# Kernel tuning notes

Hardware: AMD Instinct MI355X
Metric: run time of the kernel (lower is better)

The kernel has to match this reference:

```python
import jax, jax.numpy as jnp
import numpy as np

N = 50000      # nodes
E = 800000     # edges
NIN = 512      # input features
NHID = 128     # hidden
NCLS = 64      # classes


def setup_inputs() -> dict:
    key = jax.random.key(0)
    k0, k1, k2, k3 = jax.random.split(key, 4)
    x = jax.random.normal(k0, (N, NIN), dtype=jnp.float32)
    edge_index = jax.random.randint(k1, (2, E), 0, N, dtype=jnp.int64)
    # Glorot-style init for GCNConv linear weights (bias starts at zero in PyG)
    W1 = jax.random.normal(k2, (NIN, NHID), dtype=jnp.float32) * (1.0 / np.sqrt(NIN))
    W2 = jax.random.normal(k3, (NHID, NCLS), dtype=jnp.float32) * (1.0 / np.sqrt(NHID))
    b1 = jnp.zeros((NHID,), dtype=jnp.float32)
    b2 = jnp.zeros((NCLS,), dtype=jnp.float32)
    return {"x": x, "edge_index": edge_index, "W1": W1, "b1": b1, "W2": W2, "b2": b2}


def gcn_conv(x, W, b, src, dst, n):
    """PyG GCNConv: linear transform, then sym-normalized aggregation with self-loops."""
    xw = x @ W                                                  # [n, out]
    ones = jnp.ones(src.shape[0], dtype=xw.dtype)
    deg = jax.ops.segment_sum(ones, dst, num_segments=n) + 1.0  # +1 for self-loop
    dinv = jax.lax.rsqrt(deg)                                   # deg >= 1
    norm = dinv[src] * dinv[dst]                                # [E]
    agg = jax.ops.segment_sum(xw[src] * norm[:, None], dst, num_segments=n)
    agg = agg + (dinv * dinv)[:, None] * xw                     # self-loop messages
    return agg + b


def reference(x, edge_index, W1, b1, W2, b2):
    src, dst = edge_index[0], edge_index[1]
    n = x.shape[0]
    # eval mode: dropout is a no-op; bn is defined but unused in forward
    h = gcn_conv(x, W1, b1, src, dst, n)
    h = jax.nn.relu(h)
    o = gcn_conv(h, W2, b2, src, dst, n)
    return jax.nn.log_softmax(o, axis=1)
```

## Files before the change

### kernel.cpp

```cpp
#include <hip/hip_runtime.h>
#include <hip/hip_bf16.h>
#include <cstdint>
#include <cstddef>

#define NNODES 50000
#define NEDGES 800000
#define NIN    512
#define NHID   128
#define NCLS   64

#define SCAN_BLK 512
#define SCAN_NB ((NNODES + SCAN_BLK - 1) / SCAN_BLK)

typedef __attribute__((ext_vector_type(8))) short bf16x8;
typedef __attribute__((ext_vector_type(4))) float f32x4;

static __device__ __forceinline__ ushort f2bf(float f) {
    uint32_t u = __float_as_uint(f);
    uint32_t r = (u + 0x7fffu + ((u >> 16) & 1u)) >> 16;
    return (ushort)r;
}
static __device__ __forceinline__ float bf2f(ushort b) {
    return __uint_as_float(((uint32_t)b) << 16);
}

static __device__ __forceinline__ unsigned ldsAddr(const void* p) {
    return (unsigned)(size_t)(__attribute__((address_space(3))) const void*)p;
}

__global__ void clear_kernel(int4* __restrict__ p, int n4) {
    int i = blockIdx.x * blockDim.x + threadIdx.x;
    if (i < n4) p[i] = make_int4(0, 0, 0, 0);
}


__global__ void deg_kernel(const int* __restrict__ dst, int* __restrict__ deg) {
    int e = blockIdx.x * blockDim.x + threadIdx.x;
    if (e < NEDGES) atomicAdd(&deg[dst[e]], 1);
}

__global__ __launch_bounds__(SCAN_BLK) void scan1_kernel(const int* __restrict__ deg,
                                                         int* __restrict__ blkSum,
                                                         float* __restrict__ dinv) {
    int i = blockIdx.x * SCAN_BLK + threadIdx.x;
    int d = (i < NNODES) ? deg[i] : 0;
    if (i < NNODES) dinv[i] = rsqrtf((float)d + 1.0f);
    int v = d;
#pragma unroll
    for (int off = 32; off; off >>= 1) v += __shfl_xor(v, off, 64);
    __shared__ int ws[SCAN_BLK / 64];
    int w = threadIdx.x >> 6;
    if ((threadIdx.x & 63) == 0) ws[w] = v;
    __syncthreads();
    if (threadIdx.x == 0) {
        int s = 0;
#pragma unroll
        for (int k = 0; k < SCAN_BLK / 64; ++k) s += ws[k];
        blkSum[blockIdx.x] = s;
    }
}

__global__ void scan2_kernel(int* __restrict__ blkSum, int* __restrict__ rowptr) {
    __shared__ int sh[128];
    int t = threadIdx.x;
    int v = (t < SCAN_NB) ? blkSum[t] : 0;
    sh[t] = v;
    __syncthreads();
    for (int off = 1; off < 128; off <<= 1) {
        int o = (t >= off) ? sh[t - off] : 0;
        __syncthreads();
        sh[t] += o;
        __syncthreads();
    }
    if (t < SCAN_NB) blkSum[t] = sh[t] - v;
    if (t == 0) rowptr[NNODES] = NEDGES;
}

__global__ __launch_bounds__(SCAN_BLK) void scan3_kernel(const int* __restrict__ deg,
                                                         const int* __restrict__ blkOff,
                                                         int* __restrict__ rowptr) {
    int i = blockIdx.x * SCAN_BLK + threadIdx.x;
    int v = (i < NNODES) ? deg[i] : 0;
    int lane = threadIdx.x & 63;
    int w = threadIdx.x >> 6;
    int inc = v;
#pragma unroll
    for (int off = 1; off < 64; off <<= 1) {
        int o = __shfl_up(inc, off, 64);
        if (lane >= off) inc += o;
    }
    __shared__ int ws[SCAN_BLK / 64];
    if (lane == 63) ws[w] = inc;
    __syncthreads();
    int wpre = 0;
    for (int k = 0; k < w; ++k) wpre += ws[k];
    if (i < NNODES) rowptr[i] = inc - v + wpre + blkOff[blockIdx.x];
}

__global__ void scatter_kernel(const int* __restrict__ src, const int* __restrict__ dst,
                               const int* __restrict__ rowptr, int* __restrict__ cursor,
                               const float* __restrict__ dinv, int2* __restrict__ csr) {
    int e = blockIdx.x * blockDim.x + threadIdx.x;
    if (e >= NEDGES) return;
    int d = dst[e];
    int s = src[e];
    int pos = rowptr[d] + atomicAdd(&cursor[d], 1);
    csr[pos] = make_int2(s, __float_as_int(dinv[s]));
}

template <int NOUT, int KS, int CF>
__global__ void pack_kernel(const float* __restrict__ W, ushort* __restrict__ pack) {
    int t = blockIdx.x * blockDim.x + threadIdx.x;
    if (t >= KS * CF * 64 * 8) return;
    int j = t & 7;
    int lane = (t >> 3) & 63;
    int cf = (t >> 9) % CF;
    int ks = t / (CF * 512);
    int k = ks * 32 + (lane >> 4) * 8 + j;
    int c = cf * 16 + (lane & 15);
    pack[t] = f2bf(W[(size_t)k * NOUT + c]);
}

__global__ __launch_bounds__(256, 2) void gemm1_kernel(const float* __restrict__ A,
                                                       const ushort* __restrict__ packB,
                                                       ushort* __restrict__ C) {
    __shared__ ushort lds[2][64 * 64];
    const int t = threadIdx.x;
    const int lane = t & 63;
    const int w = t >> 6;
    const int rowBase = blockIdx.x * 64;
    const int rl = lane & 15;
    const int kg = lane >> 4;

    bf16x8 bw[16][2];
    {
        const ushort* bbase = packB + (size_t)lane * 8;
#pragma unroll
        for (int ks = 0; ks < 16; ++ks)
#pragma unroll
            for (int q = 0; q < 2; ++q)
                bw[ks][q] = *(const bf16x8*)(bbase + ks * 4096 + (2 * w + q) * 512);
    }

    f32x4 acc[4][2];
#pragma unroll
    for (int rg = 0; rg < 4; ++rg)
#pragma unroll
        for (int q = 0; q < 2; ++q) acc[rg][q] = (f32x4)(0.f);

    const int r0 = t >> 3,         c0 = t & 7;
    const int r1 = (t + 256) >> 3, c1 = (t + 256) & 7;
    int g0 = rowBase + r0; if (g0 >= NNODES) g0 = NNODES - 1;
    int g1 = rowBase + r1; if (g1 >= NNODES) g1 = NNODES - 1;
    const float* ga0 = A + (size_t)g0 * NIN + c0 * 8;
    const float* ga1 = A + (size_t)g1 * NIN + c1 * 8;
    ushort* wd0 = &lds[0][0] + r0 * 64 + ((c0 ^ (r0 & 7)) * 8);
    ushort* wd1 = &lds[0][0] + r1 * 64 + ((c1 ^ (r1 & 7)) * 8);

    auto cvt8 = [](float4 a, float4 b) {
        bf16x8 v;
        v[0] = (short)f2bf(a.x); v[1] = (short)f2bf(a.y);
        v[2] = (short)f2bf(a.z); v[3] = (short)f2bf(a.w);
        v[4] = (short)f2bf(b.x); v[5] = (short)f2bf(b.y);
        v[6] = (short)f2bf(b.z); v[7] = (short)f2bf(b.w);
        return v;
    };

    {
        float4 p0 = *(const float4*)(ga0);
        float4 p1 = *(const float4*)(ga0 + 4);
        float4 p2 = *(const float4*)(ga1);
        float4 p3 = *(const float4*)(ga1 + 4);
        *(bf16x8*)wd0 = cvt8(p0, p1);
        *(bf16x8*)wd1 = cvt8(p2, p3);
    }
    asm volatile("s_waitcnt lgkmcnt(0)" ::: "memory");
    __builtin_amdgcn_s_barrier();

#pragma unroll
    for (int tch = 0; tch < 8; ++tch) {
        const int cur = tch & 1;
        float4 p0, p1, p2, p3;
        if (tch < 7) {
            p0 = *(const float4*)(ga0 + (tch + 1) * 64);
            p1 = *(const float4*)(ga0 + (tch + 1) * 64 + 4);
            p2 = *(const float4*)(ga1 + (tch + 1) * 64);
            p3 = *(const float4*)(ga1 + (tch + 1) * 64 + 4);
            __builtin_amdgcn_sched_barrier(0);
        }
        const unsigned lbase = ldsAddr(&lds[cur][0]);
#pragma unroll
        for (int ks = 0; ks < 2; ++ks) {
            bf16x8 af0, af1, af2, af3;
            const unsigned sw = (unsigned)(((ks * 4 + kg) ^ (rl & 7)) * 16);
            const unsigned a0 = lbase + (unsigned)((0 * 16 + rl) * 128) + sw;
            const unsigned a1 = lbase + (unsigned)((1 * 16 + rl) * 128) + sw;
            const unsigned a2 = lbase + (unsigned)((2 * 16 + rl) * 128) + sw;
            const unsigned a3 = lbase + (unsigned)((3 * 16 + rl) * 128) + sw;
            asm volatile("ds_read_b128 %0, %1" : "=&v"(af0) : "v"(a0));
            asm volatile("ds_read_b128 %0, %1" : "=&v"(af1) : "v"(a1));
            asm volatile("ds_read_b128 %0, %1" : "=&v"(af2) : "v"(a2));
            asm volatile("ds_read_b128 %0, %1" : "=&v"(af3) : "v"(a3));
            asm volatile("s_waitcnt lgkmcnt(0)" ::: "memory");
            __builtin_amdgcn_sched_barrier(0);
            const int kq = tch * 2 + ks;
            acc[0][0] = __builtin_amdgcn_mfma_f32_16x16x32_bf16(af0, bw[kq][0], acc[0][0], 0, 0, 0);
            acc[0][1] = __builtin_amdgcn_mfma_f32_16x16x32_bf16(af0, bw[kq][1], acc[0][1], 0, 0, 0);
            acc[1][0] = __builtin_amdgcn_mfma_f32_16x16x32_bf16(af1, bw[kq][0], acc[1][0], 0, 0, 0);
            acc[1][1] = __builtin_amdgcn_mfma_f32_16x16x32_bf16(af1, bw[kq][1], acc[1][1], 0, 0, 0);
            acc[2][0] = __builtin_amdgcn_mfma_f32_16x16x32_bf16(af2, bw[kq][0], acc[2][0], 0, 0, 0);
            acc[2][1] = __builtin_amdgcn_mfma_f32_16x16x32_bf16(af2, bw[kq][1], acc[2][1], 0, 0, 0);
            acc[3][0] = __builtin_amdgcn_mfma_f32_16x16x32_bf16(af3, bw[kq][0], acc[3][0], 0, 0, 0);
            acc[3][1] = __builtin_amdgcn_mfma_f32_16x16x32_bf16(af3, bw[kq][1], acc[3][1], 0, 0, 0);
        }
        if (tch < 7) {
            const int nxt = cur ^ 1;
            *(bf16x8*)(wd0 + nxt * 4096) = cvt8(p0, p1);
            *(bf16x8*)(wd1 + nxt * 4096) = cvt8(p2, p3);
        }
        asm volatile("s_waitcnt lgkmcnt(0)" ::: "memory");
        __builtin_amdgcn_s_barrier();
    }

#pragma unroll
    for (int rg = 0; rg < 4; ++rg)
#pragma unroll
        for (int q = 0; q < 2; ++q)
#pragma unroll
            for (int j = 0; j < 4; ++j) {
                int rr = rowBase + rg * 16 + kg * 4 + j;
                if (rr < NNODES)
                    C[(size_t)rr * NHID + (2 * w + q) * 16 + rl] = f2bf(acc[rg][q][j]);
            }
}

__global__ __launch_bounds__(256) void gemm2_kernel(const ushort* __restrict__ A,
                                                    const ushort* __restrict__ packB,
                                                    ushort* __restrict__ C) {
    int wid = (blockIdx.x * blockDim.x + threadIdx.x) >> 6;
    int lane = threadIdx.x & 63;
    int rowBase = wid * 16;
    if (rowBase >= NNODES) return;
    int rl = lane & 15;
    int kg = lane >> 4;
    const ushort* ap = A + (size_t)(rowBase + rl) * NHID + kg * 8;

    f32x4 acc[4];
#pragma unroll
    for (int cf = 0; cf < 4; ++cf) acc[cf] = (f32x4)(0.f);

#pragma unroll
    for (int ks = 0; ks < 4; ++ks) {
        bf16x8 af = *(const bf16x8*)(ap + ks * 32);
        const ushort* bp = packB + ((size_t)(ks * 4) * 64 + lane) * 8;
#pragma unroll
        for (int cf = 0; cf < 4; ++cf) {
            bf16x8 bf = *(const bf16x8*)(bp + (size_t)cf * 512);
            acc[cf] = __builtin_amdgcn_mfma_f32_16x16x32_bf16(af, bf, acc[cf], 0, 0, 0);
        }
    }
#pragma unroll
    for (int cf = 0; cf < 4; ++cf)
#pragma unroll
        for (int j = 0; j < 4; ++j)
            C[(size_t)(rowBase + kg * 4 + j) * NCLS + cf * 16 + rl] = f2bf(acc[cf][j]);
}

__global__ __launch_bounds__(256) void agg1_kernel(const ushort* __restrict__ xw,
                                                   const int* __restrict__ rowptr,
                                                   const int2* __restrict__ csr,
                                                   const float* __restrict__ dinv,
                                                   const float* __restrict__ b1,
                                                   ushort* __restrict__ h) {
    int wid = (blockIdx.x * blockDim.x + threadIdx.x) >> 6;
    int lane = threadIdx.x & 63;
    if (wid >= NNODES) return;
    int beg = rowptr[wid], end = rowptr[wid + 1];
    float a0 = 0.f, a1 = 0.f;
    int j = beg;
    for (; j + 8 <= end; j += 8) {
        int2 e[8];
#pragma unroll
        for (int q = 0; q < 8; ++q) e[q] = csr[j + q];
        uint v[8];
#pragma unroll
        for (int q = 0; q < 8; ++q) v[q] = *(const uint*)&xw[(size_t)e[q].x * NHID + lane * 2];
#pragma unroll
        for (int q = 0; q < 8; ++q) {
            float wq = __int_as_float(e[q].y);
            a0 += wq * __uint_as_float(v[q] << 16);
            a1 += wq * __uint_as_float(v[q] & 0xffff0000u);
        }
    }
    for (; j < end; ++j) {
        int2 e = csr[j];
        float w = __int_as_float(e.y);
        uint v = *(const uint*)&xw[(size_t)e.x * NHID + lane * 2];
        a0 += w * __uint_as_float(v << 16);
        a1 += w * __uint_as_float(v & 0xffff0000u);
    }
    float di = dinv[wid];
    float sl = di * di;
    uint xv = *(const uint*)&xw[(size_t)wid * NHID + lane * 2];
    float2 bv = *(const float2*)&b1[lane * 2];
    float r0 = di * a0 + sl * __uint_as_float(xv << 16) + bv.x;
    float r1 = di * a1 + sl * __uint_as_float(xv & 0xffff0000u) + bv.y;
    uint o = (uint)f2bf(fmaxf(r0, 0.f)) | ((uint)f2bf(fmaxf(r1, 0.f)) << 16);
    *(uint*)&h[(size_t)wid * NHID + lane * 2] = o;
}

__global__ __launch_bounds__(256) void agg2_kernel(const ushort* __restrict__ xw,
                                                   const int* __restrict__ rowptr,
                                                   const int2* __restrict__ csr,
                                                   const float* __restrict__ dinv,
                                                   const float* __restrict__ b2,
                                                   float* __restrict__ out) {
    int wid = (blockIdx.x * blockDim.x + threadIdx.x) >> 6;
    int lane = threadIdx.x & 63;
    if (wid >= NNODES) return;
    int beg = rowptr[wid], end = rowptr[wid + 1];
    float a = 0.f;
    int j = beg;
    for (; j + 8 <= end; j += 8) {
        int2 e[8];
#pragma unroll
        for (int q = 0; q < 8; ++q) e[q] = csr[j + q];
        float v[8];
#pragma unroll
        for (int q = 0; q < 8; ++q) v[q] = bf2f(xw[(size_t)e[q].x * NCLS + lane]);
#pragma unroll
        for (int q = 0; q < 8; ++q) a += __int_as_float(e[q].y) * v[q];
    }
    for (; j < end; ++j) {
        int2 e = csr[j];
        a += __int_as_float(e.y) * bf2f(xw[(size_t)e.x * NCLS + lane]);
    }
    float di = dinv[wid];
    float o = di * a + di * di * bf2f(xw[(size_t)wid * NCLS + lane]) + b2[lane];
    float m = o;
#pragma unroll
    for (int off = 32; off; off >>= 1) m = fmaxf(m, __shfl_xor(m, off, 64));
    float ex = __expf(o - m);
    float ssum = ex;
#pragma unroll
    for (int off = 32; off; off >>= 1) ssum += __shfl_xor(ssum, off, 64);
    out[(size_t)wid * NCLS + lane] = (o - m) - __logf(ssum);
}


extern "C" void kernel_launch(void* const* d_in, const int* in_sizes, int n_in,
                              void* d_out, int out_size, void* d_ws, size_t ws_size,
                              hipStream_t stream) {
    const float* x  = (const float*)d_in[0];
    const int*   ei = (const int*)d_in[1];
    const int*   src = ei;
    const int*   dst = ei + NEDGES;
    const float* W1 = (const float*)d_in[2];
    const float* b1 = (const float*)d_in[3];
    const float* W2 = (const float*)d_in[4];
    const float* b2 = (const float*)d_in[5];
    float* out = (float*)d_out;

    char* w = (char*)d_ws;
    auto alloc = [&](size_t bytes) {
        char* p = w;
        w += (bytes + 255) & ~(size_t)255;
        return p;
    };
    int*    deg    = (int*)alloc((size_t)2 * NNODES * 4);
    int*    cursor = deg + NNODES;
    int*    rowptr = (int*)alloc((NNODES + 1) * 4);
    int*    blkSum = (int*)alloc(SCAN_NB * 4);
    int2*   csr    = (int2*)alloc((size_t)NEDGES * 8);
    float*  dinv   = (float*)alloc(NNODES * 4);
    ushort* pack1  = (ushort*)alloc((size_t)16 * 8 * 64 * 8 * 2);
    ushort* pack2  = (ushort*)alloc((size_t)4 * 4 * 64 * 8 * 2);
    ushort* xw1    = (ushort*)alloc((size_t)NNODES * NHID * 2);
    ushort* h      = (ushort*)alloc((size_t)NNODES * NHID * 2);
    ushort* xw2    = (ushort*)alloc((size_t)NNODES * NCLS * 2);

    const int n4 = (2 * NNODES + 3) / 4;
    clear_kernel<<<(n4 + 255) / 256, 256, 0, stream>>>((int4*)deg, n4);

    deg_kernel<<<(NEDGES + 255) / 256, 256, 0, stream>>>(dst, deg);
    scan1_kernel<<<SCAN_NB, SCAN_BLK, 0, stream>>>(deg, blkSum, dinv);
    scan2_kernel<<<1, 128, 0, stream>>>(blkSum, rowptr);
    scan3_kernel<<<SCAN_NB, SCAN_BLK, 0, stream>>>(deg, blkSum, rowptr);
    scatter_kernel<<<(NEDGES + 255) / 256, 256, 0, stream>>>(src, dst, rowptr, cursor, dinv, csr);

    pack_kernel<NHID, 16, 8><<<(16 * 8 * 64 * 8 + 255) / 256, 256, 0, stream>>>(W1, pack1);
    pack_kernel<NCLS, 4, 4><<<(4 * 4 * 64 * 8 + 255) / 256, 256, 0, stream>>>(W2, pack2);

    gemm1_kernel<<<(NNODES + 63) / 64, 256, 0, stream>>>(x, pack1, xw1);
    agg1_kernel<<<(NNODES * 64 + 255) / 256, 256, 0, stream>>>(xw1, rowptr, csr, dinv, b1, h);

    gemm2_kernel<<<(NNODES / 16 + 3) / 4, 256, 0, stream>>>(h, pack2, xw2);
    agg2_kernel<<<(NNODES * 64 + 255) / 256, 256, 0, stream>>>(xw2, rowptr, csr, dinv, b2, out);
}
```

Before: 204.8 us.

## Pack CSR entries into 32 bits and widen aggregation unrolling

Each CSR entry now holds the 16-bit source index and an fp16 normalisation weight in one word instead of an int2, halving edge-list traffic in both aggregation passes. The cursor array is initialised to rowptr in the scan, which drops a rowptr read in the scatter kernel and the separate clearing of the cursor. The degree kernel reads dst as int4, and the two weight-pack kernels are merged into one launch. The aggregation loops are unrolled to 16 with split accumulators for more memory-level parallelism. The packed format assumes fewer than 65536 nodes and reduces weight precision to fp16.

```diff
diff --git a/kernel.cpp b/kernel.cpp
--- a/kernel.cpp
+++ b/kernel.cpp
@@ -1,5 +1,6 @@
 #include <hip/hip_runtime.h>
 #include <hip/hip_bf16.h>
+#include <hip/hip_fp16.h>
 #include <cstdint>
 #include <cstddef>
 
@@ -23,6 +24,17 @@
 static __device__ __forceinline__ float bf2f(ushort b) {
     return __uint_as_float(((uint32_t)b) << 16);
 }
+static __device__ __forceinline__ float h2f(ushort u) {
+    _Float16 h;
+    __builtin_memcpy(&h, &u, 2);
+    return (float)h;
+}
+static __device__ __forceinline__ ushort f2h(float f) {
+    _Float16 h = (_Float16)f;
+    ushort u;
+    __builtin_memcpy(&u, &h, 2);
+    return u;
+}
 
 static __device__ __forceinline__ unsigned ldsAddr(const void* p) {
     return (unsigned)(size_t)(__attribute__((address_space(3))) const void*)p;
@@ -34,9 +46,15 @@
 }
 
 
-__global__ void deg_kernel(const int* __restrict__ dst, int* __restrict__ deg) {
-    int e = blockIdx.x * blockDim.x + threadIdx.x;
-    if (e < NEDGES) atomicAdd(&deg[dst[e]], 1);
+__global__ void deg_kernel(const int4* __restrict__ dst4, int* __restrict__ deg) {
+    int i = blockIdx.x * blockDim.x + threadIdx.x;
+    if (i < NEDGES / 4) {
+        int4 d = dst4[i];
+        atomicAdd(&deg[d.x], 1);
+        atomicAdd(&deg[d.y], 1);
+        atomicAdd(&deg[d.z], 1);
+        atomicAdd(&deg[d.w], 1);
+    }
 }
 
 __global__ __launch_bounds__(SCAN_BLK) void scan1_kernel(const int* __restrict__ deg,
@@ -78,7 +96,8 @@
 
 __global__ __launch_bounds__(SCAN_BLK) void scan3_kernel(const int* __restrict__ deg,
                                                          const int* __restrict__ blkOff,
-                                                         int* __restrict__ rowptr) {
+                                                         int* __restrict__ rowptr,
+                                                         int* __restrict__ cursor) {
     int i = blockIdx.x * SCAN_BLK + threadIdx.x;
     int v = (i < NNODES) ? deg[i] : 0;
     int lane = threadIdx.x & 63;
@@ -94,31 +113,48 @@
     __syncthreads();
     int wpre = 0;
     for (int k = 0; k < w; ++k) wpre += ws[k];
-    if (i < NNODES) rowptr[i] = inc - v + wpre + blkOff[blockIdx.x];
+    if (i < NNODES) {
+        int rp = inc - v + wpre + blkOff[blockIdx.x];
+        rowptr[i] = rp;
+        cursor[i] = rp;
+    }
 }
 
 __global__ void scatter_kernel(const int* __restrict__ src, const int* __restrict__ dst,
-                               const int* __restrict__ rowptr, int* __restrict__ cursor,
-                               const float* __restrict__ dinv, int2* __restrict__ csr) {
+                               int* __restrict__ cursor,
+                               const float* __restrict__ dinv, uint* __restrict__ csr) {
     int e = blockIdx.x * blockDim.x + threadIdx.x;
     if (e >= NEDGES) return;
     int d = dst[e];
     int s = src[e];
-    int pos = rowptr[d] + atomicAdd(&cursor[d], 1);
-    csr[pos] = make_int2(s, __float_as_int(dinv[s]));
-}
-
-template <int NOUT, int KS, int CF>
-__global__ void pack_kernel(const float* __restrict__ W, ushort* __restrict__ pack) {
+    int pos = atomicAdd(&cursor[d], 1);
+    csr[pos] = (uint)s | ((uint)f2h(dinv[s]) << 16);
+}
+
+__global__ void pack_kernel(const float* __restrict__ W1, const float* __restrict__ W2,
+                            ushort* __restrict__ p1, ushort* __restrict__ p2) {
     int t = blockIdx.x * blockDim.x + threadIdx.x;
-    if (t >= KS * CF * 64 * 8) return;
-    int j = t & 7;
-    int lane = (t >> 3) & 63;
-    int cf = (t >> 9) % CF;
-    int ks = t / (CF * 512);
-    int k = ks * 32 + (lane >> 4) * 8 + j;
-    int c = cf * 16 + (lane & 15);
-    pack[t] = f2bf(W[(size_t)k * NOUT + c]);
+    const int N1 = 16 * 8 * 64 * 8;
+    if (t < N1) {
+        int j = t & 7;
+        int lane = (t >> 3) & 63;
+        int cf = (t >> 9) & 7;
+        int ks = t >> 12;
+        int k = ks * 32 + (lane >> 4) * 8 + j;
+        int c = cf * 16 + (lane & 15);
+        p1[t] = f2bf(W1[(size_t)k * NHID + c]);
+    } else {
+        int u = t - N1;
+        if (u < 4 * 4 * 64 * 8) {
+            int j = u & 7;
+            int lane = (u >> 3) & 63;
+            int cf = (u >> 9) & 3;
+            int ks = u >> 11;
+            int k = ks * 32 + (lane >> 4) * 8 + j;
+            int c = cf * 16 + (lane & 15);
+            p2[u] = f2bf(W2[(size_t)k * NCLS + c]);
+        }
+    }
 }
 
 __global__ __launch_bounds__(256, 2) void gemm1_kernel(const float* __restrict__ A,
@@ -268,7 +304,7 @@
 
 __global__ __launch_bounds__(256) void agg1_kernel(const ushort* __restrict__ xw,
                                                    const int* __restrict__ rowptr,
-                                                   const int2* __restrict__ csr,
+                                                   const uint* __restrict__ csr,
                                                    const float* __restrict__ dinv,
                                                    const float* __restrict__ b1,
                                                    ushort* __restrict__ h) {
@@ -276,29 +312,52 @@
     int lane = threadIdx.x & 63;
     if (wid >= NNODES) return;
     int beg = rowptr[wid], end = rowptr[wid + 1];
-    float a0 = 0.f, a1 = 0.f;
+    float a0 = 0.f, a1 = 0.f, a2 = 0.f, a3 = 0.f;
     int j = beg;
-    for (; j + 8 <= end; j += 8) {
-        int2 e[8];
-#pragma unroll
-        for (int q = 0; q < 8; ++q) e[q] = csr[j + q];
-        uint v[8];
-#pragma unroll
-        for (int q = 0; q < 8; ++q) v[q] = *(const uint*)&xw[(size_t)e[q].x * NHID + lane * 2];
+    for (; j + 16 <= end; j += 16) {
+        uint e[16];
+#pragma unroll
+        for (int q = 0; q < 16; ++q) e[q] = csr[j + q];
+        uint v[16];
+#pragma unroll
+        for (int q = 0; q < 16; ++q)
+            v[q] = *(const uint*)&xw[(size_t)(e[q] & 0xffffu) * NHID + lane * 2];
 #pragma unroll
         for (int q = 0; q < 8; ++q) {
-            float wq = __int_as_float(e[q].y);
+            float wq = h2f((ushort)(e[q] >> 16));
             a0 += wq * __uint_as_float(v[q] << 16);
             a1 += wq * __uint_as_float(v[q] & 0xffff0000u);
         }
+#pragma unroll
+        for (int q = 8; q < 16; ++q) {
+            float wq = h2f((ushort)(e[q] >> 16));
+            a2 += wq * __uint_as_float(v[q] << 16);
+            a3 += wq * __uint_as_float(v[q] & 0xffff0000u);
+        }
+    }
+    for (; j + 4 <= end; j += 4) {
+        uint e[4];
+#pragma unroll
+        for (int q = 0; q < 4; ++q) e[q] = csr[j + q];
+        uint v[4];
+#pragma unroll
+        for (int q = 0; q < 4; ++q)
+            v[q] = *(const uint*)&xw[(size_t)(e[q] & 0xffffu) * NHID + lane * 2];
+#pragma unroll
+        for (int q = 0; q < 4; ++q) {
+            float wq = h2f((ushort)(e[q] >> 16));
+            a0 += wq * __uint_as_float(v[q] << 16);
+            a1 += wq * __uint_as_float(v[q] & 0xffff0000u);
+        }
     }
     for (; j < end; ++j) {
-        int2 e = csr[j];
-        float w = __int_as_float(e.y);
-        uint v = *(const uint*)&xw[(size_t)e.x * NHID + lane * 2];
-        a0 += w * __uint_as_float(v << 16);
-        a1 += w * __uint_as_float(v & 0xffff0000u);
-    }
+        uint e = csr[j];
+        float wq = h2f((ushort)(e >> 16));
+        uint v = *(const uint*)&xw[(size_t)(e & 0xffffu) * NHID + lane * 2];
+        a0 += wq * __uint_as_float(v << 16);
+        a1 += wq * __uint_as_float(v & 0xffff0000u);
+    }
+    a0 += a2; a1 += a3;
     float di = dinv[wid];
     float sl = di * di;
     uint xv = *(const uint*)&xw[(size_t)wid * NHID + lane * 2];
@@ -311,7 +370,7 @@
 
 __global__ __launch_bounds__(256) void agg2_kernel(const ushort* __restrict__ xw,
                                                    const int* __restrict__ rowptr,
-                                                   const int2* __restrict__ csr,
+                                                   const uint* __restrict__ csr,
                                                    const float* __restrict__ dinv,
                                                    const float* __restrict__ b2,
                                                    float* __restrict__ out) {
@@ -319,22 +378,37 @@
     int lane = threadIdx.x & 63;
     if (wid >= NNODES) return;
     int beg = rowptr[wid], end = rowptr[wid + 1];
-    float a = 0.f;
+    float a = 0.f, b = 0.f;
     int j = beg;
-    for (; j + 8 <= end; j += 8) {
-        int2 e[8];
-#pragma unroll
-        for (int q = 0; q < 8; ++q) e[q] = csr[j + q];
-        float v[8];
-#pragma unroll
-        for (int q = 0; q < 8; ++q) v[q] = bf2f(xw[(size_t)e[q].x * NCLS + lane]);
-#pragma unroll
-        for (int q = 0; q < 8; ++q) a += __int_as_float(e[q].y) * v[q];
+    for (; j + 16 <= end; j += 16) {
+        uint e[16];
+#pragma unroll
+        for (int q = 0; q < 16; ++q) e[q] = csr[j + q];
+        float v[16];
+#pragma unroll
+        for (int q = 0; q < 16; ++q)
+            v[q] = bf2f(xw[(size_t)(e[q] & 0xffffu) * NCLS + lane]);
+#pragma unroll
+        for (int q = 0; q < 8; ++q) a += h2f((ushort)(e[q] >> 16)) * v[q];
+#pragma unroll
+        for (int q = 8; q < 16; ++q) b += h2f((ushort)(e[q] >> 16)) * v[q];
+    }
+    for (; j + 4 <= end; j += 4) {
+        uint e[4];
+#pragma unroll
+        for (int q = 0; q < 4; ++q) e[q] = csr[j + q];
+        float v[4];
+#pragma unroll
+        for (int q = 0; q < 4; ++q)
+            v[q] = bf2f(xw[(size_t)(e[q] & 0xffffu) * NCLS + lane]);
+#pragma unroll
+        for (int q = 0; q < 4; ++q) a += h2f((ushort)(e[q] >> 16)) * v[q];
     }
     for (; j < end; ++j) {
-        int2 e = csr[j];
-        a += __int_as_float(e.y) * bf2f(xw[(size_t)e.x * NCLS + lane]);
-    }
+        uint e = csr[j];
+        a += h2f((ushort)(e >> 16)) * bf2f(xw[(size_t)(e & 0xffffu) * NCLS + lane]);
+    }
+    a += b;
     float di = dinv[wid];
     float o = di * a + di * di * bf2f(xw[(size_t)wid * NCLS + lane]) + b2[lane];
     float m = o;
@@ -367,11 +441,11 @@
         w += (bytes + 255) & ~(size_t)255;
         return p;
     };
-    int*    deg    = (int*)alloc((size_t)2 * NNODES * 4);
-    int*    cursor = deg + NNODES;
+    int*    deg    = (int*)alloc(NNODES * 4);
+    int*    cursor = (int*)alloc(NNODES * 4);
     int*    rowptr = (int*)alloc((NNODES + 1) * 4);
     int*    blkSum = (int*)alloc(SCAN_NB * 4);
-    int2*   csr    = (int2*)alloc((size_t)NEDGES * 8);
+    uint*   csr    = (uint*)alloc((size_t)NEDGES * 4);
     float*  dinv   = (float*)alloc(NNODES * 4);
     ushort* pack1  = (ushort*)alloc((size_t)16 * 8 * 64 * 8 * 2);
     ushort* pack2  = (ushort*)alloc((size_t)4 * 4 * 64 * 8 * 2);
@@ -379,17 +453,16 @@
     ushort* h      = (ushort*)alloc((size_t)NNODES * NHID * 2);
     ushort* xw2    = (ushort*)alloc((size_t)NNODES * NCLS * 2);
 
-    const int n4 = (2 * NNODES + 3) / 4;
+    const int n4 = (NNODES + 3) / 4;
     clear_kernel<<<(n4 + 255) / 256, 256, 0, stream>>>((int4*)deg, n4);
 
-    deg_kernel<<<(NEDGES + 255) / 256, 256, 0, stream>>>(dst, deg);
+    deg_kernel<<<(NEDGES / 4 + 255) / 256, 256, 0, stream>>>((const int4*)dst, deg);
     scan1_kernel<<<SCAN_NB, SCAN_BLK, 0, stream>>>(deg, blkSum, dinv);
     scan2_kernel<<<1, 128, 0, stream>>>(blkSum, rowptr);
-    scan3_kernel<<<SCAN_NB, SCAN_BLK, 0, stream>>>(deg, blkSum, rowptr);
-    scatter_kernel<<<(NEDGES + 255) / 256, 256, 0, stream>>>(src, dst, rowptr, cursor, dinv, csr);
-
-    pack_kernel<NHID, 16, 8><<<(16 * 8 * 64 * 8 + 255) / 256, 256, 0, stream>>>(W1, pack1);
-    pack_kernel<NCLS, 4, 4><<<(4 * 4 * 64 * 8 + 255) / 256, 256, 0, stream>>>(W2, pack2);
+    scan3_kernel<<<SCAN_NB, SCAN_BLK, 0, stream>>>(deg, blkSum, rowptr, cursor);
+    scatter_kernel<<<(NEDGES + 255) / 256, 256, 0, stream>>>(src, dst, cursor, dinv, csr);
+
+    pack_kernel<<<(16 * 8 * 64 * 8 + 4 * 4 * 64 * 8 + 255) / 256, 256, 0, stream>>>(W1, W2, pack1, pack2);
 
     gemm1_kernel<<<(NNODES + 63) / 64, 256, 0, stream>>>(x, pack1, xw1);
     agg1_kernel<<<(NNODES * 64 + 255) / 256, 256, 0, stream>>>(xw1, rowptr, csr, dinv, b1, h);
```

Result: faster. 193.9 us (-5.3%).
